# Kernel optimization log

Hardware: AMD Instinct MI355X
Metric: run time of the kernel (lower is better)

Reference implementation:

```python
import jax, jax.numpy as jnp
import numpy as np

B, N, D_IN, D_OUT = 16, 2048, 128, 128

def setup_inputs() -> dict:
    key = jax.random.key(0)
    ks = jax.random.split(key, 8)
    x = jax.random.normal(ks[0], (B, N, D_IN), dtype=jnp.float32)
    adj = jax.random.randint(ks[1], (N, N), 0, 2).astype(jnp.float32)
    # Conv1d(kernel_size=1) weights, PyTorch default uniform init scale
    s_emb = 1.0 / np.sqrt(D_IN)
    W_emb = jax.random.uniform(ks[2], (D_OUT, D_IN), jnp.float32, -s_emb, s_emb)
    b_emb = jax.random.uniform(ks[3], (D_OUT,), jnp.float32, -s_emb, s_emb)
    s_qk = 1.0 / np.sqrt(D_OUT)
    w_q = jax.random.uniform(ks[4], (D_OUT,), jnp.float32, -s_qk, s_qk)
    b_q = jax.random.uniform(ks[5], (1,), jnp.float32, -s_qk, s_qk)
    w_k = jax.random.uniform(ks[6], (D_OUT,), jnp.float32, -s_qk, s_qk)
    b_k = jax.random.uniform(ks[7], (1,), jnp.float32, -s_qk, s_qk)
    return {"x": x, "adj": adj, "W_emb": W_emb, "b_emb": b_emb,
            "w_q": w_q, "b_q": b_q, "w_k": w_k, "b_k": b_k}

def reference(x, adj, W_emb, b_emb, w_q, b_q, w_k, b_k):
    # emb_conv: 1x1 conv over node dim == per-node linear  [B,N,D_out]
    seq_fts = jnp.einsum('bni,oi->bno', x, W_emb) + b_emb
    # q_conv / k_conv: project to scalar per node  [B,N]
    q = jnp.einsum('bnd,d->bn', seq_fts, w_q) + b_q  # f_1_t squeezed
    k = jnp.einsum('bnd,d->bn', seq_fts, w_k) + b_k  # f_2_t squeezed
    # f[b,i,j] = f_1_t[b,0,j] + f_2_t^T[b,i,0] = q[b,j] + k[b,i]
    f = k[:, :, None] + q[:, None, :]                 # [B,N,N]
    f = jax.nn.leaky_relu(adj[None, :, :] * f, negative_slope=0.01)
    coefs = jax.nn.softmax(f, axis=1)                 # softmax over dim=1 (rows)
    vals = jnp.einsum('bij,bjd->bid', coefs, seq_fts)  # [B,N,D_out]
    return vals
```

## Files before the change

### kernel.cpp

```cpp
#include <hip/hip_runtime.h>
#include <hip/hip_bf16.h>
#include <stdint.h>

#define B_ 16
#define N_ 2048
#define D_ 128

typedef __bf16 bf16_t;
typedef bf16_t bf16x8 __attribute__((ext_vector_type(8)));
typedef float f32x4 __attribute__((ext_vector_type(4)));

__global__ __launch_bounds__(256, 2) void k_emb(const float* __restrict__ x,
                                                const float* __restrict__ W,
                                                const float* __restrict__ be,
                                                const float* __restrict__ wq,
                                                const float* __restrict__ bq,
                                                const float* __restrict__ wk,
                                                const float* __restrict__ bk,
                                                const float* __restrict__ adj,
                                                unsigned int* __restrict__ bits,
                                                bf16_t* __restrict__ Pb,
                                                float* __restrict__ qa, float* __restrict__ ka,
                                                float* __restrict__ Eq, float* __restrict__ eqs,
                                                float* __restrict__ Ek, float* __restrict__ eks) {
    __shared__ float xs[32][68];
    __shared__ float ws[32][132];
    __shared__ float qs[64], ks[64];
    int b  = blockIdx.y;
    int n0 = blockIdx.x * 64;
    int tid = threadIdx.x;
    int tx = tid & 15, ty = tid >> 4;
    if (tid < 64) { qs[tid] = 0.f; ks[tid] = 0.f; }

    {
        int base = (blockIdx.y * (N_ / 64) + blockIdx.x) * 256 + tid;
#pragma unroll 8
        for (int it = 0; it < (N_ * N_) / (512 * 256); ++it) {
            int t = base + it * (512 * 256);
            float v = adj[t];
            unsigned long long m = __ballot(v > 0.5f);
            if ((t & 63) == 0) {
                int i = t >> 11;
                int j = t & 2047;
                bits[i * 64 + (j >> 5)]     = (unsigned int)m;
                bits[i * 64 + (j >> 5) + 1] = (unsigned int)(m >> 32);
            }
        }
    }

    float acc[4][8] = {};
    f32x4 xr[2], wr[4];

    auto loadregs = [&](int kc) {
#pragma unroll
        for (int s = 0; s < 2; ++s) {
            int p = tid + 256 * s;
            int n = p >> 3, kq = p & 7;
            xr[s] = *(const f32x4*)(x + ((size_t)(b * N_ + n0 + n)) * D_ + kc * 32 + kq * 4);
        }
#pragma unroll
        for (int s = 0; s < 4; ++s) {
            int p = tid + 256 * s;
            int d = p >> 3, kq = p & 7;
            wr[s] = *(const f32x4*)(W + (size_t)d * D_ + kc * 32 + kq * 4);
        }
    };
    auto writelds = [&]() {
#pragma unroll
        for (int s = 0; s < 2; ++s) {
            int p = tid + 256 * s;
            int n = p >> 3, kq = p & 7;
#pragma unroll
            for (int u = 0; u < 4; ++u) xs[kq * 4 + u][n] = xr[s][u];
        }
#pragma unroll
        for (int s = 0; s < 4; ++s) {
            int p = tid + 256 * s;
            int d = p >> 3, kq = p & 7;
#pragma unroll
            for (int u = 0; u < 4; ++u) ws[kq * 4 + u][d] = wr[s][u];
        }
    };

    loadregs(0);
    for (int kc = 0; kc < 4; ++kc) {
        writelds();
        __syncthreads();
        if (kc < 3) loadregs(kc + 1);
#pragma unroll 4
        for (int k = 0; k < 32; ++k) {
            f32x4 xv  = *(const f32x4*)&xs[k][tx * 4];
            f32x4 wv0 = *(const f32x4*)&ws[k][ty * 8];
            f32x4 wv1 = *(const f32x4*)&ws[k][ty * 8 + 4];
#pragma unroll
            for (int i = 0; i < 4; ++i)
#pragma unroll
                for (int j = 0; j < 8; ++j)
                    acc[i][j] += xv[i] * ((j < 4) ? wv0[j] : wv1[j - 4]);
        }
        __syncthreads();
    }

    float qp[4] = {}, kp[4] = {};
#pragma unroll
    for (int j = 0; j < 8; ++j) {
        int d = ty * 8 + j;
        float bj  = be[d];
        float wqj = wq[d];
        float wkj = wk[d];
        f32x4 o;
        bf16_t ob[4];
#pragma unroll
        for (int i = 0; i < 4; ++i) {
            o[i] = acc[i][j] + bj;
            qp[i] += o[i] * wqj;
            kp[i] += o[i] * wkj;
            ob[i] = (bf16_t)o[i];
        }
        *(uint2*)(Pb + ((size_t)b * D_ + d) * N_ + n0 + tx * 4) = *(uint2*)ob;
    }
#pragma unroll
    for (int i = 0; i < 4; ++i) {
        atomicAdd(&qs[tx * 4 + i], qp[i]);
        atomicAdd(&ks[tx * 4 + i], kp[i]);
    }
    __syncthreads();
    if (tid < 64) {
        int idx = b * N_ + n0 + tid;
        float aq = qs[tid] + bq[0];
        float ak = ks[tid] + bk[0];
        qa[idx] = aq;          ka[idx] = ak;
        Eq[idx] = expf(aq);    eqs[idx] = expf(0.01f * aq);
        Ek[idx] = expf(ak);    eks[idx] = expf(0.01f * ak);
    }
}

__global__ __launch_bounds__(1024) void k_denom(const unsigned int* __restrict__ bits,
                                                const float* __restrict__ qa,
                                                const float* __restrict__ ka,
                                                const float* __restrict__ Eq,
                                                const float* __restrict__ eqs,
                                                const float* __restrict__ Ek,
                                                const float* __restrict__ eks,
                                                float* __restrict__ rd,
                                                float* __restrict__ Eqr,
                                                float* __restrict__ eqr) {
    __shared__ float red[8][128];
    int jt  = blockIdx.x;
    int b   = blockIdx.y;
    int tid = threadIdx.x;
    int tj  = tid & 127;
    int sg  = tid >> 7;
    int j   = jt * 128 + tj;
    float qj  = qa[b * N_ + j];
    float Eqj = Eq[b * N_ + j];
    float eqj = eqs[b * N_ + j];
    int shift = j & 31;
    int wid   = j >> 5;
    float acc = 0.f;
    int i0 = sg * 256;
#pragma unroll 16
    for (int i = i0; i < i0 + 256; ++i) {
        float kk  = ka[b * N_ + i];
        float Ekk = Ek[b * N_ + i];
        float ekk = eks[b * N_ + i];
        unsigned int w = bits[i * 64 + wid];
        float z  = kk + qj;
        float f1 = z > 0.f ? Ekk : ekk;
        float f2 = z > 0.f ? Eqj : eqj;
        acc += ((w >> shift) & 1u) ? f1 * f2 : 1.0f;
    }
    red[sg][tj] = acc;
    __syncthreads();
    if (sg == 0) {
        float den = acc;
#pragma unroll
        for (int s = 1; s < 8; ++s) den += red[s][tj];
        float r = 1.0f / den;
        int idx = b * N_ + j;
        rd[idx]  = r;
        Eqr[idx] = Eqj * r;
        eqr[idx] = eqj * r;
    }
}

__global__ __launch_bounds__(256, 2) void k_attn(const float* __restrict__ qa,
                                                 const float* __restrict__ ka,
                                                 const float* __restrict__ Ek,
                                                 const float* __restrict__ eks,
                                                 const float* __restrict__ rd,
                                                 const float* __restrict__ Eqr,
                                                 const float* __restrict__ eqr,
                                                 const unsigned int* __restrict__ bits,
                                                 const bf16_t* __restrict__ Pb,
                                                 float* __restrict__ out) {
    __shared__ __align__(16) bf16_t ldsB[2][128 * 64];
    __shared__ __align__(16) bf16_t ldsA[2][4 * 2 * 64 * 8];
    int n     = blockIdx.x;
    int xcd   = n & 7;
    int slot  = n >> 3;
    int b     = xcd * 2 + (slot >> 5);
    int ibase = (slot & 31) * 64;
    int tid   = threadIdx.x;
    int w     = tid >> 6;
    int lane  = tid & 63;
    int m16   = lane & 15;
    int quad  = lane >> 4;
    int ig    = w & 1;
    int dg    = w >> 1;

    int iA = ibase + (2 * ig) * 16 + m16;
    int iB = iA + 16;
    float mkR0 = -ka[b * N_ + iA], mkR1 = -ka[b * N_ + iB];
    float EkR0 = Ek[b * N_ + iA],  EkR1 = Ek[b * N_ + iB];
    float ekR0 = eks[b * N_ + iA], ekR1 = eks[b * N_ + iB];
    const unsigned int* brA = bits + (size_t)iA * 64;
    const unsigned int* brB = bits + (size_t)iB * 64;
    const float* qp  = qa  + b * N_;
    const float* Erp = Eqr + b * N_;
    const float* erp = eqr + b * N_;
    const float* rdp = rd  + b * N_;
    const bf16_t* PtB = Pb + (size_t)b * D_ * N_;

    f32x4 acc[2][4];
#pragma unroll
    for (int c = 0; c < 2; ++c)
#pragma unroll
        for (int nt = 0; nt < 4; ++nt) acc[c][nt] = (f32x4){0.f, 0.f, 0.f, 0.f};

    f32x4 qv4[2][2], Er4[2][2], er4[2][2], rd4[2][2];
    unsigned int mA[2], mB[2];

    auto ldj = [&](int par, int jb) {
        int j0 = jb + dg * 32 + quad * 8;
        qv4[par][0] = *(const f32x4*)(qp  + j0);
        qv4[par][1] = *(const f32x4*)(qp  + j0 + 4);
        Er4[par][0] = *(const f32x4*)(Erp + j0);
        Er4[par][1] = *(const f32x4*)(Erp + j0 + 4);
        er4[par][0] = *(const f32x4*)(erp + j0);
        er4[par][1] = *(const f32x4*)(erp + j0 + 4);
        rd4[par][0] = *(const f32x4*)(rdp + j0);
        rd4[par][1] = *(const f32x4*)(rdp + j0 + 4);
        mA[par] = brA[(jb >> 5) + dg];
        mB[par] = brB[(jb >> 5) + dg];
    };

    auto stage = [&](int bufi, int jb) {
#pragma unroll
        for (int t = 0; t < 4; ++t) {
            int off = t * 4096 + tid * 16;
            int d   = off >> 7;
            int g   = ((off & 127) >> 4) ^ (d & 7);
            const bf16_t* gp = PtB + (size_t)d * N_ + jb + g * 8;
            __builtin_amdgcn_global_load_lds(
                (const __attribute__((address_space(1))) void*)gp,
                (__attribute__((address_space(3))) void*)((char*)(&ldsB[bufi][0]) + off),
                16, 0, 0);
        }
    };

    auto agen = [&](int par, bf16x8& afA, bf16x8& afB) {
#pragma unroll
        for (int t = 0; t < 8; ++t) {
            float qv = (t < 4) ? qv4[par][0][t] : qv4[par][1][t - 4];
            float Er = (t < 4) ? Er4[par][0][t] : Er4[par][1][t - 4];
            float er = (t < 4) ? er4[par][0][t] : er4[par][1][t - 4];
            float rj = (t < 4) ? rd4[par][0][t] : rd4[par][1][t - 4];
            int bit = quad * 8 + t;
            {
                bool c = qv > mkR0;
                float v = (c ? EkR0 : ekR0) * (c ? Er : er);
                afA[t] = (bf16_t)(((mA[par] >> bit) & 1u) ? v : rj);
            }
            {
                bool c = qv > mkR1;
                float v = (c ? EkR1 : ekR1) * (c ? Er : er);
                afB[t] = (bf16_t)(((mB[par] >> bit) & 1u) ? v : rj);
            }
        }
        *(bf16x8*)((char*)&ldsA[par][0] + ((((2 * ig + 0) * 2 + dg) * 64 + lane) * 16)) = afA;
        *(bf16x8*)((char*)&ldsA[par][0] + ((((2 * ig + 1) * 2 + dg) * 64 + lane) * 16)) = afB;
    };

    auto mfma_phase = [&](int buf, int par, const bf16x8& afA, const bf16x8& afB) {
        {
            int cph = ((dg * 4 + quad) ^ (m16 & 7)) * 8;
#pragma unroll
            for (int nt = 0; nt < 4; ++nt) {
                int d = dg * 64 + nt * 16 + m16;
                bf16x8 bf = *(const bf16x8*)&ldsB[buf][d * 64 + cph];
                acc[0][nt] = __builtin_amdgcn_mfma_f32_16x16x32_bf16(afA, bf, acc[0][nt], 0, 0, 0);
                acc[1][nt] = __builtin_amdgcn_mfma_f32_16x16x32_bf16(afB, bf, acc[1][nt], 0, 0, 0);
            }
        }
        {
            int oh = 1 - dg;
            bf16x8 a0 = *(const bf16x8*)((char*)&ldsA[par][0] + ((((2 * ig + 0) * 2 + oh) * 64 + lane) * 16));
            bf16x8 a1 = *(const bf16x8*)((char*)&ldsA[par][0] + ((((2 * ig + 1) * 2 + oh) * 64 + lane) * 16));
            int cph = ((oh * 4 + quad) ^ (m16 & 7)) * 8;
#pragma unroll
            for (int nt = 0; nt < 4; ++nt) {
                int d = dg * 64 + nt * 16 + m16;
                bf16x8 bf = *(const bf16x8*)&ldsB[buf][d * 64 + cph];
                acc[0][nt] = __builtin_amdgcn_mfma_f32_16x16x32_bf16(a0, bf, acc[0][nt], 0, 0, 0);
                acc[1][nt] = __builtin_amdgcn_mfma_f32_16x16x32_bf16(a1, bf, acc[1][nt], 0, 0, 0);
            }
        }
    };

    stage(0, 0);
    ldj(0, 0);
    int buf = 0;
#pragma unroll 1
    for (int s2 = 0; s2 < 15; ++s2) {
#pragma unroll
        for (int par = 0; par < 2; ++par) {
            int jb = (s2 * 2 + par) * 64;

            bf16x8 afA, afB;
            agen(par, afA, afB);
            asm volatile("s_waitcnt vmcnt(0) lgkmcnt(0)" ::: "memory");
            __builtin_amdgcn_s_barrier();

            ldj(par ^ 1, jb + 64);
            stage(buf ^ 1, jb + 64);

            __builtin_amdgcn_s_setprio(1);
            mfma_phase(buf, par, afA, afB);
            __builtin_amdgcn_s_setprio(0);
            buf ^= 1;
        }
    }
    {
        bf16x8 afA, afB;
        agen(0, afA, afB);
        asm volatile("s_waitcnt vmcnt(0) lgkmcnt(0)" ::: "memory");
        __builtin_amdgcn_s_barrier();
        ldj(1, 31 * 64);
        stage(buf ^ 1, 31 * 64);
        __builtin_amdgcn_s_setprio(1);
        mfma_phase(buf, 0, afA, afB);
        __builtin_amdgcn_s_setprio(0);
        buf ^= 1;
    }
    {
        bf16x8 afA, afB;
        agen(1, afA, afB);
        asm volatile("s_waitcnt vmcnt(0) lgkmcnt(0)" ::: "memory");
        __builtin_amdgcn_s_barrier();
        __builtin_amdgcn_s_setprio(1);
        mfma_phase(buf, 1, afA, afB);
        __builtin_amdgcn_s_setprio(0);
    }

#pragma unroll
    for (int c = 0; c < 2; ++c) {
        int irow = ibase + (2 * ig + c) * 16 + quad * 4;
#pragma unroll
        for (int nt = 0; nt < 4; ++nt) {
            int d = dg * 64 + nt * 16 + m16;
#pragma unroll
            for (int r = 0; r < 4; ++r)
                out[((size_t)b * N_ + irow + r) * D_ + d] = acc[c][nt][r];
        }
    }
}

extern "C" void kernel_launch(void* const* d_in, const int* in_sizes, int n_in,
                              void* d_out, int out_size, void* d_ws, size_t ws_size,
                              hipStream_t stream) {
    const float* x   = (const float*)d_in[0];
    const float* adj = (const float*)d_in[1];
    const float* W   = (const float*)d_in[2];
    const float* be  = (const float*)d_in[3];
    const float* wq  = (const float*)d_in[4];
    const float* bq  = (const float*)d_in[5];
    const float* wk  = (const float*)d_in[6];
    const float* bk  = (const float*)d_in[7];
    float* out = (float*)d_out;

    char* ws = (char*)d_ws;
    size_t off = 0;
    bf16_t* Pb = (bf16_t*)(ws + off); off += (size_t)B_ * D_ * N_ * 2;
    float* qa  = (float*)(ws + off);  off += (size_t)B_ * N_ * 4;
    float* ka  = (float*)(ws + off);  off += (size_t)B_ * N_ * 4;
    float* Eq  = (float*)(ws + off);  off += (size_t)B_ * N_ * 4;
    float* eqs = (float*)(ws + off);  off += (size_t)B_ * N_ * 4;
    float* Ek  = (float*)(ws + off);  off += (size_t)B_ * N_ * 4;
    float* eks = (float*)(ws + off);  off += (size_t)B_ * N_ * 4;
    float* rd  = (float*)(ws + off);  off += (size_t)B_ * N_ * 4;
    float* Eqr = (float*)(ws + off);  off += (size_t)B_ * N_ * 4;
    float* eqr = (float*)(ws + off);  off += (size_t)B_ * N_ * 4;
    unsigned int* bits = (unsigned int*)(ws + off); off += (size_t)N_ * 64 * 4;

    k_emb<<<dim3(N_ / 64, B_), 256, 0, stream>>>(x, W, be, wq, bq, wk, bk,
                                                 adj, bits,
                                                 Pb, qa, ka, Eq, eqs, Ek, eks);
    k_denom<<<dim3(16, 16), 1024, 0, stream>>>(bits, qa, ka, Eq, eqs, Ek, eks,
                                               rd, Eqr, eqr);
    k_attn<<<512, 256, 0, stream>>>(qa, ka, Ek, eks, rd, Eqr, eqr,
                                    bits, Pb, out);
}
```

Measured before the change: 196.7 us.

## Overlap A-fragment generation with MFMA and issue prefetch before barrier

```diff
diff --git a/kernel.cpp b/kernel.cpp
--- a/kernel.cpp
+++ b/kernel.cpp
@@ -228,21 +228,21 @@
 #pragma unroll
         for (int nt = 0; nt < 4; ++nt) acc[c][nt] = (f32x4){0.f, 0.f, 0.f, 0.f};
 
-    f32x4 qv4[2][2], Er4[2][2], er4[2][2], rd4[2][2];
-    unsigned int mA[2], mB[2];
-
-    auto ldj = [&](int par, int jb) {
+    f32x4 qv4[2], Er4[2], er4[2], rd4[2];
+    unsigned int mA, mB;
+
+    auto ldj = [&](int jb) {
         int j0 = jb + dg * 32 + quad * 8;
-        qv4[par][0] = *(const f32x4*)(qp  + j0);
-        qv4[par][1] = *(const f32x4*)(qp  + j0 + 4);
-        Er4[par][0] = *(const f32x4*)(Erp + j0);
-        Er4[par][1] = *(const f32x4*)(Erp + j0 + 4);
-        er4[par][0] = *(const f32x4*)(erp + j0);
-        er4[par][1] = *(const f32x4*)(erp + j0 + 4);
-        rd4[par][0] = *(const f32x4*)(rdp + j0);
-        rd4[par][1] = *(const f32x4*)(rdp + j0 + 4);
-        mA[par] = brA[(jb >> 5) + dg];
-        mB[par] = brB[(jb >> 5) + dg];
+        qv4[0] = *(const f32x4*)(qp  + j0);
+        qv4[1] = *(const f32x4*)(qp  + j0 + 4);
+        Er4[0] = *(const f32x4*)(Erp + j0);
+        Er4[1] = *(const f32x4*)(Erp + j0 + 4);
+        er4[0] = *(const f32x4*)(erp + j0);
+        er4[1] = *(const f32x4*)(erp + j0 + 4);
+        rd4[0] = *(const f32x4*)(rdp + j0);
+        rd4[1] = *(const f32x4*)(rdp + j0 + 4);
+        mA = brA[(jb >> 5) + dg];
+        mB = brB[(jb >> 5) + dg];
     };
 
     auto stage = [&](int bufi, int jb) {
@@ -259,25 +259,28 @@
         }
     };
 
-    auto agen = [&](int par, bf16x8& afA, bf16x8& afB) {
+    auto agen = [&](bf16x8& afA, bf16x8& afB) {
 #pragma unroll
         for (int t = 0; t < 8; ++t) {
-            float qv = (t < 4) ? qv4[par][0][t] : qv4[par][1][t - 4];
-            float Er = (t < 4) ? Er4[par][0][t] : Er4[par][1][t - 4];
-            float er = (t < 4) ? er4[par][0][t] : er4[par][1][t - 4];
-            float rj = (t < 4) ? rd4[par][0][t] : rd4[par][1][t - 4];
+            float qv = (t < 4) ? qv4[0][t] : qv4[1][t - 4];
+            float Er = (t < 4) ? Er4[0][t] : Er4[1][t - 4];
+            float er = (t < 4) ? er4[0][t] : er4[1][t - 4];
+            float rj = (t < 4) ? rd4[0][t] : rd4[1][t - 4];
             int bit = quad * 8 + t;
             {
                 bool c = qv > mkR0;
                 float v = (c ? EkR0 : ekR0) * (c ? Er : er);
-                afA[t] = (bf16_t)(((mA[par] >> bit) & 1u) ? v : rj);
+                afA[t] = (bf16_t)(((mA >> bit) & 1u) ? v : rj);
             }
             {
                 bool c = qv > mkR1;
                 float v = (c ? EkR1 : ekR1) * (c ? Er : er);
-                afB[t] = (bf16_t)(((mB[par] >> bit) & 1u) ? v : rj);
+                afB[t] = (bf16_t)(((mB >> bit) & 1u) ? v : rj);
             }
         }
+    };
+
+    auto publish = [&](int par, const bf16x8& afA, const bf16x8& afB) {
         *(bf16x8*)((char*)&ldsA[par][0] + ((((2 * ig + 0) * 2 + dg) * 64 + lane) * 16)) = afA;
         *(bf16x8*)((char*)&ldsA[par][0] + ((((2 * ig + 1) * 2 + dg) * 64 + lane) * 16)) = afB;
     };
@@ -308,8 +311,10 @@
         }
     };
 
+    bf16x8 afA, afB;
+    ldj(0);
     stage(0, 0);
-    ldj(0, 0);
+    agen(afA, afB);
     int buf = 0;
 #pragma unroll 1
     for (int s2 = 0; s2 < 15; ++s2) {
@@ -317,35 +322,42 @@
         for (int par = 0; par < 2; ++par) {
             int jb = (s2 * 2 + par) * 64;
 
-            bf16x8 afA, afB;
-            agen(par, afA, afB);
-            asm volatile("s_waitcnt vmcnt(0) lgkmcnt(0)" ::: "memory");
+            publish(par, afA, afB);
+            ldj(jb + 64);
+            stage(buf ^ 1, jb + 64);
+            asm volatile("s_waitcnt vmcnt(14) lgkmcnt(0)" ::: "memory");
             __builtin_amdgcn_s_barrier();
 
-            ldj(par ^ 1, jb + 64);
-            stage(buf ^ 1, jb + 64);
-
+            bf16x8 nA, nB;
             __builtin_amdgcn_s_setprio(1);
             mfma_phase(buf, par, afA, afB);
             __builtin_amdgcn_s_setprio(0);
+            agen(nA, nB);
+            afA = nA; afB = nB;
+
+            asm volatile("s_waitcnt lgkmcnt(0)" ::: "memory");
+            __builtin_amdgcn_s_barrier();
             buf ^= 1;
         }
     }
     {
-        bf16x8 afA, afB;
-        agen(0, afA, afB);
-        asm volatile("s_waitcnt vmcnt(0) lgkmcnt(0)" ::: "memory");
+        publish(0, afA, afB);
+        ldj(31 * 64);
+        stage(buf ^ 1, 31 * 64);
+        asm volatile("s_waitcnt vmcnt(14) lgkmcnt(0)" ::: "memory");
         __builtin_amdgcn_s_barrier();
-        ldj(1, 31 * 64);
-        stage(buf ^ 1, 31 * 64);
+        bf16x8 nA, nB;
         __builtin_amdgcn_s_setprio(1);
         mfma_phase(buf, 0, afA, afB);
         __builtin_amdgcn_s_setprio(0);
+        agen(nA, nB);
+        afA = nA; afB = nB;
+        asm volatile("s_waitcnt lgkmcnt(0)" ::: "memory");
+        __builtin_amdgcn_s_barrier();
         buf ^= 1;
     }
     {
-        bf16x8 afA, afB;
-        agen(1, afA, afB);
+        publish(1, afA, afB);
         asm volatile("s_waitcnt vmcnt(0) lgkmcnt(0)" ::: "memory");
         __builtin_amdgcn_s_barrier();
         __builtin_amdgcn_s_setprio(1);
```

New measurement: 193.5 us. About the same (-1.7%).
